# Kernel tuning notes

Measured on AMD Instinct MI355X. Metric: run time of the kernel, lower is better.

Reference implementation:

```python
import jax, jax.numpy as jnp
import numpy as np

EMBED = 64
HEAD = 16

def setup_inputs() -> dict:
    key = jax.random.key(0)
    k1, k2, k3, k4 = jax.random.split(key, 4)
    x = jax.random.normal(k1, (4, 4096, EMBED), dtype=jnp.float32)
    # store weights as [in, out] so forward is x @ W (equivalent to torch Linear with W.T)
    Wq = jax.random.normal(k2, (EMBED, HEAD), dtype=jnp.float32) * (1.0 / np.sqrt(EMBED))
    Wk = jax.random.normal(k3, (EMBED, HEAD), dtype=jnp.float32) * (1.0 / np.sqrt(EMBED))
    Wv = jax.random.normal(k4, (EMBED, EMBED), dtype=jnp.float32) * (1.0 / np.sqrt(EMBED))
    return {"x": x, "Wq": Wq, "Wk": Wk, "Wv": Wv}

def reference(x, Wq, Wk, Wv):
    # q,k: [B,T,HEAD]; v: [B,T,EMBED]
    q = x @ Wq
    k = x @ Wk
    v = x @ Wv
    scores = jnp.einsum('bqh,bkh->bqk', q, k)  # [B,T,T]
    T = scores.shape[-1]
    # causal mask: positions with key > query set to -inf BEFORE scaling (matches original; same result)
    causal = jnp.tril(jnp.ones((T, T), dtype=bool))
    scores = jnp.where(causal, scores, -jnp.inf)
    attn = jax.nn.softmax(scores / np.sqrt(HEAD).astype(np.float32), axis=-1)
    return jnp.einsum('bqk,bkd->bqd', attn, v)  # [B,T,EMBED]
```

## Files before the change

kernel.cpp:

```cpp
#include <hip/hip_runtime.h>


#define TSEQ 4096
#define NBATCH 4

typedef __attribute__((ext_vector_type(4)))  float fvec4;
typedef __attribute__((ext_vector_type(16))) float f32x16;
typedef __attribute__((ext_vector_type(4)))  short s16x4;
typedef __attribute__((ext_vector_type(8)))  short s16x8;

union I4S8 { int i[4]; s16x8 v; };

static __device__ __forceinline__ unsigned short f2bf(float f) {
    unsigned u = __float_as_uint(f);
    u += 0x7FFFu + ((u >> 16) & 1u);
    return (unsigned short)(u >> 16);
}

static __device__ __forceinline__ int cvt_pk_bf16(float lo, float hi) {
    int r;
    asm("v_cvt_pk_bf16_f32 %0, %1, %2" : "=v"(r) : "v"(lo), "v"(hi));
    return r;
}

static __device__ __forceinline__ s16x8 cat4(s16x4 a, s16x4 b) {
    return __builtin_shufflevector(a, b, 0, 1, 2, 3, 4, 5, 6, 7);
}

__global__ __launch_bounds__(128)
__attribute__((amdgpu_waves_per_eu(2, 4)))
void proj_kernel(
    const float* __restrict__ x,  const float* __restrict__ Wq,
    const float* __restrict__ Wk, const float* __restrict__ Wv,
    unsigned short* __restrict__ qb, unsigned short* __restrict__ kb,
    unsigned short* __restrict__ vf)
{
    __shared__ float xs[64][66];
    __shared__ __align__(16) unsigned short Wh[96][76], Wl[96][76];
    const int tid  = threadIdx.x;
    const int w    = tid >> 6;
    const int lane = tid & 63;
    const int col  = lane & 31;
    const int g    = lane >> 5;

    {
        const float* xblk = x + (size_t)blockIdx.x * 64 * 64;
        #pragma unroll
        for (int j = 0; j < 8; ++j) {
            const int fi = (tid + 128 * j) * 4;
            fvec4 v = *(const fvec4*)(xblk + fi);
            const int r = fi >> 6, c = fi & 63;
            xs[r][c + 0] = v[0]; xs[r][c + 1] = v[1];
            xs[r][c + 2] = v[2]; xs[r][c + 3] = v[3];
        }
    }
    const float SCQ = 0.25f * 1.44269504088896340736f;
    #pragma unroll
    for (int j = 0; j < 8; ++j) {
        const int idx = tid + 128 * j;
        const int n = idx & 15, k = idx >> 4;
        float wv = Wq[idx] * SCQ;
        unsigned short h = f2bf(wv);
        Wh[n][k] = h;
        Wl[n][k] = f2bf(wv - __uint_as_float((unsigned)h << 16));
    }
    #pragma unroll
    for (int j = 0; j < 8; ++j) {
        const int idx = tid + 128 * j;
        const int n = idx & 15, k = idx >> 4;
        float wv = Wk[idx];
        unsigned short h = f2bf(wv);
        Wh[16 + n][k] = h;
        Wl[16 + n][k] = f2bf(wv - __uint_as_float((unsigned)h << 16));
    }
    #pragma unroll
    for (int j = 0; j < 32; ++j) {
        const int idx = tid + 128 * j;
        const int n = idx & 63, k = idx >> 6;
        float wv = Wv[idx];
        unsigned short h = f2bf(wv);
        Wh[32 + n][k] = h;
        Wl[32 + n][k] = f2bf(wv - __uint_as_float((unsigned)h << 16));
    }
    __syncthreads();

    const int row0 = blockIdx.x * 64 + w * 32;
    const int lrow = w * 32 + col;

    s16x8 xh[4], xl[4];
    #pragma unroll
    for (int kc = 0; kc < 4; ++kc) {
        const float* xp = &xs[lrow][kc * 16 + 8 * g];
        float2 a0 = *(const float2*)(xp + 0);
        float2 a1 = *(const float2*)(xp + 2);
        float2 a2 = *(const float2*)(xp + 4);
        float2 a3 = *(const float2*)(xp + 6);
        I4S8 uh, ul;
        uh.i[0] = cvt_pk_bf16(a0.x, a0.y);
        uh.i[1] = cvt_pk_bf16(a1.x, a1.y);
        uh.i[2] = cvt_pk_bf16(a2.x, a2.y);
        uh.i[3] = cvt_pk_bf16(a3.x, a3.y);
        ul.i[0] = cvt_pk_bf16(a0.x - __uint_as_float((unsigned)uh.i[0] << 16),
                              a0.y - __uint_as_float((unsigned)uh.i[0] & 0xffff0000u));
        ul.i[1] = cvt_pk_bf16(a1.x - __uint_as_float((unsigned)uh.i[1] << 16),
                              a1.y - __uint_as_float((unsigned)uh.i[1] & 0xffff0000u));
        ul.i[2] = cvt_pk_bf16(a2.x - __uint_as_float((unsigned)uh.i[2] << 16),
                              a2.y - __uint_as_float((unsigned)uh.i[2] & 0xffff0000u));
        ul.i[3] = cvt_pk_bf16(a3.x - __uint_as_float((unsigned)uh.i[3] << 16),
                              a3.y - __uint_as_float((unsigned)uh.i[3] & 0xffff0000u));
        xh[kc] = uh.v; xl[kc] = ul.v;
    }

    f32x16 acc0 = (f32x16)0.0f, acc1 = (f32x16)0.0f, acc2 = (f32x16)0.0f;
    #pragma unroll
    for (int nt = 0; nt < 3; ++nt) {
        const int n = nt * 32 + col;
        f32x16 a = nt == 0 ? acc0 : (nt == 1 ? acc1 : acc2);
        #pragma unroll
        for (int kc = 0; kc < 4; ++kc) {
            const int off = kc * 16 + 8 * g;
            s16x8 bh = cat4(*(const s16x4*)&Wh[n][off], *(const s16x4*)&Wh[n][off + 4]);
            s16x8 bl = cat4(*(const s16x4*)&Wl[n][off], *(const s16x4*)&Wl[n][off + 4]);
            a = __builtin_amdgcn_mfma_f32_32x32x16_bf16(xh[kc], bh, a, 0, 0, 0);
            a = __builtin_amdgcn_mfma_f32_32x32x16_bf16(xl[kc], bh, a, 0, 0, 0);
            a = __builtin_amdgcn_mfma_f32_32x32x16_bf16(xh[kc], bl, a, 0, 0, 0);
        }
        if (nt == 0) acc0 = a; else if (nt == 1) acc1 = a; else acc2 = a;
    }

    {
        unsigned short* dst = (col < 16) ? (qb + col) : (kb + (col - 16));
        #pragma unroll
        for (int rr = 0; rr < 16; ++rr) {
            const int grow = row0 + (rr & 3) + 8 * (rr >> 2) + 4 * g;
            dst[(size_t)grow * 16] = f2bf(acc0[rr]);
        }
    }
    {
        unsigned short* const vtile = vf + (size_t)blockIdx.x * 4096;
        #pragma unroll
        for (int mt = 0; mt < 2; ++mt) {
            const f32x16 a = mt ? acc2 : acc1;
            #pragma unroll
            for (int ci = 0; ci < 2; ++ci) {
                I4S8 pk;
                pk.i[0] = cvt_pk_bf16(a[8*ci + 0], a[8*ci + 1]);
                pk.i[1] = cvt_pk_bf16(a[8*ci + 2], a[8*ci + 3]);
                pk.i[2] = cvt_pk_bf16(a[8*ci + 4], a[8*ci + 5]);
                pk.i[3] = cvt_pk_bf16(a[8*ci + 6], a[8*ci + 7]);
                const int c = 2 * w + ci;
                *(s16x8*)(vtile + ((c * 2 + mt) * 64 + lane) * 8) = pk.v;
            }
        }
    }
}

template<bool DIAG>
static __device__ __forceinline__ void do_tile32(
    const unsigned short* kp, const unsigned short* vt, const int lane,
    const s16x8 qf, const int col, const int g,
    f32x16& o0, f32x16& o1, float& lsum)
{
    s16x8 kf   = *(const s16x8*)(kp);
    s16x8 va00 = *(const s16x8*)(vt + (0 * 64 + lane) * 8);
    s16x8 va01 = *(const s16x8*)(vt + (1 * 64 + lane) * 8);
    s16x8 va10 = *(const s16x8*)(vt + (2 * 64 + lane) * 8);
    s16x8 va11 = *(const s16x8*)(vt + (3 * 64 + lane) * 8);

    f32x16 s = __builtin_amdgcn_mfma_f32_32x32x16_bf16(kf, qf, (f32x16)0.0f, 0, 0, 0);

    float psA = 0.f, psB = 0.f;
    #pragma unroll
    for (int rr = 0; rr < 16; ++rr) {
        float ev = __builtin_amdgcn_exp2f(s[rr]);
        if (DIAG) {
            const int drow = (rr & 3) + 8 * (rr >> 2) + 4 * g;
            ev = (drow <= col) ? ev : 0.f;
        }
        s[rr] = ev;
        if (rr & 1) psB += ev; else psA += ev;
    }
    lsum += psA + psB;

    I4S8 pa, pb;
    pa.i[0] = cvt_pk_bf16(s[0],  s[1]);
    pa.i[1] = cvt_pk_bf16(s[2],  s[3]);
    pa.i[2] = cvt_pk_bf16(s[4],  s[5]);
    pa.i[3] = cvt_pk_bf16(s[6],  s[7]);
    pb.i[0] = cvt_pk_bf16(s[8],  s[9]);
    pb.i[1] = cvt_pk_bf16(s[10], s[11]);
    pb.i[2] = cvt_pk_bf16(s[12], s[13]);
    pb.i[3] = cvt_pk_bf16(s[14], s[15]);

    o0 = __builtin_amdgcn_mfma_f32_32x32x16_bf16(va00, pa.v, o0, 0, 0, 0);
    o1 = __builtin_amdgcn_mfma_f32_32x32x16_bf16(va01, pa.v, o1, 0, 0, 0);
    o0 = __builtin_amdgcn_mfma_f32_32x32x16_bf16(va10, pb.v, o0, 0, 0, 0);
    o1 = __builtin_amdgcn_mfma_f32_32x32x16_bf16(va11, pb.v, o1, 0, 0, 0);
}

__global__ __launch_bounds__(1024)
__attribute__((amdgpu_num_vgpr(128), amdgpu_waves_per_eu(4, 4)))
void attn_kernel(
    const unsigned short* __restrict__ qb, const unsigned short* __restrict__ kb,
    const unsigned short* __restrict__ vf, float* __restrict__ out)
{
    __shared__ float pl[16][32];
    __shared__ float pO[2048 * 17];
    __shared__ float outS[32][66];

    const int tid  = threadIdx.x;
    const int w    = tid >> 6;
    const int lane = tid & 63;
    const int col  = lane & 31;
    const int g    = lane >> 5;
    const int b    = blockIdx.y;
    const int p    = blockIdx.x;

    const unsigned short* const kbase = kb + (size_t)b * TSEQ * 16 + (size_t)col * 16 + 8 * g;
    const unsigned short* const vbase = vf + (size_t)b * 64 * 4096;

    for (int half = 0; half < 2; ++half) {
        const int i  = half ? (127 - p) : p;
        const int q0 = i * 32;

        const s16x8 qf = *(const s16x8*)(qb + ((size_t)(b * TSEQ) + q0 + col) * 16 + 8 * g);

        f32x16 o0 = (f32x16)0.0f, o1 = (f32x16)0.0f;
        float lsum = 0.f;

        int t = w;
        for (; t < i; t += 16) {
            do_tile32<false>(kbase + (size_t)t * 512,
                             vbase + (size_t)(t >> 1) * 4096 + (t & 1) * 2048,
                             lane, qf, col, g, o0, o1, lsum);
        }
        if (t == i) {
            do_tile32<true>(kbase + (size_t)t * 512,
                            vbase + (size_t)(t >> 1) * 4096 + (t & 1) * 2048,
                            lane, qf, col, g, o0, o1, lsum);
        }
        lsum += __shfl_xor(lsum, 32);

        if (g == 0) pl[w][col] = lsum;
        #pragma unroll
        for (int mt = 0; mt < 2; ++mt) {
            const f32x16 oa = mt ? o1 : o0;
            #pragma unroll
            for (int rr = 0; rr < 16; ++rr) {
                const int dv = mt * 32 + (rr & 3) + 8 * (rr >> 2) + 4 * g;
                pO[(dv * 32 + col) * 17 + w] = oa[rr];
            }
        }
        __syncthreads();

        {
            const int q   = tid & 31;
            const int dvh = tid >> 5;
            float L = 0.f;
            #pragma unroll
            for (int ww = 0; ww < 16; ++ww) L += pl[ww][q];
            const float inv = 1.0f / L;
            #pragma unroll
            for (int pass = 0; pass < 2; ++pass) {
                const int dv = dvh + 32 * pass;
                const float* prow = &pO[(dv * 32 + q) * 17];
                float sA = 0.f, sB = 0.f;
                #pragma unroll
                for (int c = 0; c < 8; ++c) { sA += prow[2*c]; sB += prow[2*c+1]; }
                outS[q][dv] = (sA + sB) * inv;
            }
        }
        __syncthreads();

        {
            const int q2  = tid >> 5;
            const int dvp = (tid & 31) * 2;
            float2 v2 = *(const float2*)&outS[q2][dvp];
            *(float2*)(out + ((size_t)(b * TSEQ) + q0 + q2) * 64 + dvp) = v2;
        }
    }
}

extern "C" void kernel_launch(void* const* d_in, const int* in_sizes, int n_in,
                              void* d_out, int out_size, void* d_ws, size_t ws_size,
                              hipStream_t stream) {
    const float* x  = (const float*)d_in[0];
    const float* Wq = (const float*)d_in[1];
    const float* Wk = (const float*)d_in[2];
    const float* Wv = (const float*)d_in[3];

    unsigned short* qb = (unsigned short*)d_ws;
    unsigned short* kb = qb + (size_t)NBATCH * TSEQ * 16;
    unsigned short* vf = kb + (size_t)NBATCH * TSEQ * 16;
    float* out = (float*)d_out;

    proj_kernel<<<dim3((NBATCH * TSEQ) / 64), 128, 0, stream>>>(x, Wq, Wk, Wv, qb, kb, vf);
    attn_kernel<<<dim3(64, NBATCH), 1024, 0, stream>>>(qb, kb, vf, out);
}
```

Before: 24.15 us.

## Precompute split-bf16 weight fragments in a separate prep kernel

Adds a single-block wprep_kernel that converts Wq (pre-scaled), Wk and Wv into hi/lo bf16 pairs, stored in MFMA B-fragment order in workspace. The projection kernel then loads these fragments straight from global memory into registers. This removes the per-block weight conversion, the transposed LDS stores and the LDS reads, along with about 29KB of shared memory per block, which may raise occupancy. The cost is an extra kernel launch with a serial dependency and one more global read of the weights in every block.

```diff
diff --git a/kernel.cpp b/kernel.cpp
--- a/kernel.cpp
+++ b/kernel.cpp
@@ -23,20 +23,51 @@
     return r;
 }
 
-static __device__ __forceinline__ s16x8 cat4(s16x4 a, s16x4 b) {
-    return __builtin_shufflevector(a, b, 0, 1, 2, 3, 4, 5, 6, 7);
+__global__ __launch_bounds__(256) void wprep_kernel(
+    const float* __restrict__ Wq, const float* __restrict__ Wk,
+    const float* __restrict__ Wv,
+    unsigned short* __restrict__ whf, unsigned short* __restrict__ wlf)
+{
+    const float SCQ = 0.25f * 1.44269504088896340736f;
+    const int t = threadIdx.x;
+    #pragma unroll
+    for (int j = 0; j < 3; ++j) {
+        const int r  = t + 256 * j;
+        const int ch = r >> 6;
+        const int l  = r & 63;
+        const int nt = ch >> 2, kc = ch & 3;
+        const int n  = nt * 32 + (l & 31);
+        const int k0 = kc * 16 + (l >> 5) * 8;
+        float wv[8];
+        #pragma unroll
+        for (int e = 0; e < 8; ++e) {
+            const int k = k0 + e;
+            wv[e] = (nt == 0)
+                  ? ((n < 16) ? Wq[k * 16 + n] * SCQ : Wk[k * 16 + (n - 16)])
+                  : Wv[k * 64 + (nt - 1) * 32 + (l & 31)];
+        }
+        I4S8 hi, lo;
+        #pragma unroll
+        for (int ii = 0; ii < 4; ++ii) {
+            hi.i[ii] = cvt_pk_bf16(wv[2*ii], wv[2*ii + 1]);
+            const float h0 = __uint_as_float((unsigned)hi.i[ii] << 16);
+            const float h1 = __uint_as_float((unsigned)hi.i[ii] & 0xffff0000u);
+            lo.i[ii] = cvt_pk_bf16(wv[2*ii] - h0, wv[2*ii + 1] - h1);
+        }
+        *(s16x8*)(whf + (size_t)r * 8) = hi.v;
+        *(s16x8*)(wlf + (size_t)r * 8) = lo.v;
+    }
 }
 
 __global__ __launch_bounds__(128)
 __attribute__((amdgpu_waves_per_eu(2, 4)))
 void proj_kernel(
-    const float* __restrict__ x,  const float* __restrict__ Wq,
-    const float* __restrict__ Wk, const float* __restrict__ Wv,
+    const float* __restrict__ x,
+    const unsigned short* __restrict__ whf, const unsigned short* __restrict__ wlf,
     unsigned short* __restrict__ qb, unsigned short* __restrict__ kb,
     unsigned short* __restrict__ vf)
 {
     __shared__ float xs[64][66];
-    __shared__ __align__(16) unsigned short Wh[96][76], Wl[96][76];
     const int tid  = threadIdx.x;
     const int w    = tid >> 6;
     const int lane = tid & 63;
@@ -53,34 +84,6 @@
             xs[r][c + 0] = v[0]; xs[r][c + 1] = v[1];
             xs[r][c + 2] = v[2]; xs[r][c + 3] = v[3];
         }
-    }
-    const float SCQ = 0.25f * 1.44269504088896340736f;
-    #pragma unroll
-    for (int j = 0; j < 8; ++j) {
-        const int idx = tid + 128 * j;
-        const int n = idx & 15, k = idx >> 4;
-        float wv = Wq[idx] * SCQ;
-        unsigned short h = f2bf(wv);
-        Wh[n][k] = h;
-        Wl[n][k] = f2bf(wv - __uint_as_float((unsigned)h << 16));
-    }
-    #pragma unroll
-    for (int j = 0; j < 8; ++j) {
-        const int idx = tid + 128 * j;
-        const int n = idx & 15, k = idx >> 4;
-        float wv = Wk[idx];
-        unsigned short h = f2bf(wv);
-        Wh[16 + n][k] = h;
-        Wl[16 + n][k] = f2bf(wv - __uint_as_float((unsigned)h << 16));
-    }
-    #pragma unroll
-    for (int j = 0; j < 32; ++j) {
-        const int idx = tid + 128 * j;
-        const int n = idx & 63, k = idx >> 6;
-        float wv = Wv[idx];
-        unsigned short h = f2bf(wv);
-        Wh[32 + n][k] = h;
-        Wl[32 + n][k] = f2bf(wv - __uint_as_float((unsigned)h << 16));
     }
     __syncthreads();
 
@@ -114,16 +117,19 @@
     f32x16 acc0 = (f32x16)0.0f, acc1 = (f32x16)0.0f, acc2 = (f32x16)0.0f;
     #pragma unroll
     for (int nt = 0; nt < 3; ++nt) {
-        const int n = nt * 32 + col;
         f32x16 a = nt == 0 ? acc0 : (nt == 1 ? acc1 : acc2);
+        s16x8 bh[4], bl[4];
         #pragma unroll
         for (int kc = 0; kc < 4; ++kc) {
-            const int off = kc * 16 + 8 * g;
-            s16x8 bh = cat4(*(const s16x4*)&Wh[n][off], *(const s16x4*)&Wh[n][off + 4]);
-            s16x8 bl = cat4(*(const s16x4*)&Wl[n][off], *(const s16x4*)&Wl[n][off + 4]);
-            a = __builtin_amdgcn_mfma_f32_32x32x16_bf16(xh[kc], bh, a, 0, 0, 0);
-            a = __builtin_amdgcn_mfma_f32_32x32x16_bf16(xl[kc], bh, a, 0, 0, 0);
-            a = __builtin_amdgcn_mfma_f32_32x32x16_bf16(xh[kc], bl, a, 0, 0, 0);
+            const size_t fo = ((size_t)((nt * 4 + kc) * 64 + lane)) * 8;
+            bh[kc] = *(const s16x8*)(whf + fo);
+            bl[kc] = *(const s16x8*)(wlf + fo);
+        }
+        #pragma unroll
+        for (int kc = 0; kc < 4; ++kc) {
+            a = __builtin_amdgcn_mfma_f32_32x32x16_bf16(xh[kc], bh[kc], a, 0, 0, 0);
+            a = __builtin_amdgcn_mfma_f32_32x32x16_bf16(xl[kc], bh[kc], a, 0, 0, 0);
+            a = __builtin_amdgcn_mfma_f32_32x32x16_bf16(xh[kc], bl[kc], a, 0, 0, 0);
         }
         if (nt == 0) acc0 = a; else if (nt == 1) acc1 = a; else acc2 = a;
     }
@@ -289,11 +295,14 @@
     const float* Wk = (const float*)d_in[2];
     const float* Wv = (const float*)d_in[3];
 
-    unsigned short* qb = (unsigned short*)d_ws;
-    unsigned short* kb = qb + (size_t)NBATCH * TSEQ * 16;
-    unsigned short* vf = kb + (size_t)NBATCH * TSEQ * 16;
+    unsigned short* qb  = (unsigned short*)d_ws;
+    unsigned short* kb  = qb + (size_t)NBATCH * TSEQ * 16;
+    unsigned short* vf  = kb + (size_t)NBATCH * TSEQ * 16;
+    unsigned short* whf = vf + (size_t)NBATCH * 64 * 4096;
+    unsigned short* wlf = whf + 12 * 64 * 8;
     float* out = (float*)d_out;
 
-    proj_kernel<<<dim3((NBATCH * TSEQ) / 64), 128, 0, stream>>>(x, Wq, Wk, Wv, qb, kb, vf);
+    wprep_kernel<<<1, 256, 0, stream>>>(Wq, Wk, Wv, whf, wlf);
+    proj_kernel<<<dim3((NBATCH * TSEQ) / 64), 128, 0, stream>>>(x, whf, wlf, qb, kb, vf);
     attn_kernel<<<dim3(64, NBATCH), 1024, 0, stream>>>(qb, kb, vf, out);
 }
```

Result: slower. 27.63 us (+14.4%).

## Fuse projection and attention into one cooperative kernel with grid sync

Applied to the files above, without the earlier changes.

Merges the separate projection and attention kernels into a single cooperative launch of 256 blocks of 1024 threads. Each block first computes the bf16 Q/K/V projection for its 64 rows using 6 waves, then a grid-wide sync, then runs the attention phase. Shared memory is aliased between the two phases. This removes one kernel launch and the gap between launches, at the cost of a grid barrier, idle waves during projection, and a requirement that all blocks are co-resident.

```diff
diff --git a/kernel.cpp b/kernel.cpp
--- a/kernel.cpp
+++ b/kernel.cpp
@@ -1,4 +1,7 @@
 #include <hip/hip_runtime.h>
+#include <hip/hip_cooperative_groups.h>
+
+namespace cg = cooperative_groups;
 
 
 #define TSEQ 4096
@@ -25,134 +28,6 @@
 
 static __device__ __forceinline__ s16x8 cat4(s16x4 a, s16x4 b) {
     return __builtin_shufflevector(a, b, 0, 1, 2, 3, 4, 5, 6, 7);
-}
-
-__global__ __launch_bounds__(128)
-__attribute__((amdgpu_waves_per_eu(2, 4)))
-void proj_kernel(
-    const float* __restrict__ x,  const float* __restrict__ Wq,
-    const float* __restrict__ Wk, const float* __restrict__ Wv,
-    unsigned short* __restrict__ qb, unsigned short* __restrict__ kb,
-    unsigned short* __restrict__ vf)
-{
-    __shared__ float xs[64][66];
-    __shared__ __align__(16) unsigned short Wh[96][76], Wl[96][76];
-    const int tid  = threadIdx.x;
-    const int w    = tid >> 6;
-    const int lane = tid & 63;
-    const int col  = lane & 31;
-    const int g    = lane >> 5;
-
-    {
-        const float* xblk = x + (size_t)blockIdx.x * 64 * 64;
-        #pragma unroll
-        for (int j = 0; j < 8; ++j) {
-            const int fi = (tid + 128 * j) * 4;
-            fvec4 v = *(const fvec4*)(xblk + fi);
-            const int r = fi >> 6, c = fi & 63;
-            xs[r][c + 0] = v[0]; xs[r][c + 1] = v[1];
-            xs[r][c + 2] = v[2]; xs[r][c + 3] = v[3];
-        }
-    }
-    const float SCQ = 0.25f * 1.44269504088896340736f;
-    #pragma unroll
-    for (int j = 0; j < 8; ++j) {
-        const int idx = tid + 128 * j;
-        const int n = idx & 15, k = idx >> 4;
-        float wv = Wq[idx] * SCQ;
-        unsigned short h = f2bf(wv);
-        Wh[n][k] = h;
-        Wl[n][k] = f2bf(wv - __uint_as_float((unsigned)h << 16));
-    }
-    #pragma unroll
-    for (int j = 0; j < 8; ++j) {
-        const int idx = tid + 128 * j;
-        const int n = idx & 15, k = idx >> 4;
-        float wv = Wk[idx];
-        unsigned short h = f2bf(wv);
-        Wh[16 + n][k] = h;
-        Wl[16 + n][k] = f2bf(wv - __uint_as_float((unsigned)h << 16));
-    }
-    #pragma unroll
-    for (int j = 0; j < 32; ++j) {
-        const int idx = tid + 128 * j;
-        const int n = idx & 63, k = idx >> 6;
-        float wv = Wv[idx];
-        unsigned short h = f2bf(wv);
-        Wh[32 + n][k] = h;
-        Wl[32 + n][k] = f2bf(wv - __uint_as_float((unsigned)h << 16));
-    }
-    __syncthreads();
-
-    const int row0 = blockIdx.x * 64 + w * 32;
-    const int lrow = w * 32 + col;
-
-    s16x8 xh[4], xl[4];
-    #pragma unroll
-    for (int kc = 0; kc < 4; ++kc) {
-        const float* xp = &xs[lrow][kc * 16 + 8 * g];
-        float2 a0 = *(const float2*)(xp + 0);
-        float2 a1 = *(const float2*)(xp + 2);
-        float2 a2 = *(const float2*)(xp + 4);
-        float2 a3 = *(const float2*)(xp + 6);
-        I4S8 uh, ul;
-        uh.i[0] = cvt_pk_bf16(a0.x, a0.y);
-        uh.i[1] = cvt_pk_bf16(a1.x, a1.y);
-        uh.i[2] = cvt_pk_bf16(a2.x, a2.y);
-        uh.i[3] = cvt_pk_bf16(a3.x, a3.y);
-        ul.i[0] = cvt_pk_bf16(a0.x - __uint_as_float((unsigned)uh.i[0] << 16),
-                              a0.y - __uint_as_float((unsigned)uh.i[0] & 0xffff0000u));
-        ul.i[1] = cvt_pk_bf16(a1.x - __uint_as_float((unsigned)uh.i[1] << 16),
-                              a1.y - __uint_as_float((unsigned)uh.i[1] & 0xffff0000u));
-        ul.i[2] = cvt_pk_bf16(a2.x - __uint_as_float((unsigned)uh.i[2] << 16),
-                              a2.y - __uint_as_float((unsigned)uh.i[2] & 0xffff0000u));
-        ul.i[3] = cvt_pk_bf16(a3.x - __uint_as_float((unsigned)uh.i[3] << 16),
-                              a3.y - __uint_as_float((unsigned)uh.i[3] & 0xffff0000u));
-        xh[kc] = uh.v; xl[kc] = ul.v;
-    }
-
-    f32x16 acc0 = (f32x16)0.0f, acc1 = (f32x16)0.0f, acc2 = (f32x16)0.0f;
-    #pragma unroll
-    for (int nt = 0; nt < 3; ++nt) {
-        const int n = nt * 32 + col;
-        f32x16 a = nt == 0 ? acc0 : (nt == 1 ? acc1 : acc2);
-        #pragma unroll
-        for (int kc = 0; kc < 4; ++kc) {
-            const int off = kc * 16 + 8 * g;
-            s16x8 bh = cat4(*(const s16x4*)&Wh[n][off], *(const s16x4*)&Wh[n][off + 4]);
-            s16x8 bl = cat4(*(const s16x4*)&Wl[n][off], *(const s16x4*)&Wl[n][off + 4]);
-            a = __builtin_amdgcn_mfma_f32_32x32x16_bf16(xh[kc], bh, a, 0, 0, 0);
-            a = __builtin_amdgcn_mfma_f32_32x32x16_bf16(xl[kc], bh, a, 0, 0, 0);
-            a = __builtin_amdgcn_mfma_f32_32x32x16_bf16(xh[kc], bl, a, 0, 0, 0);
-        }
-        if (nt == 0) acc0 = a; else if (nt == 1) acc1 = a; else acc2 = a;
-    }
-
-    {
-        unsigned short* dst = (col < 16) ? (qb + col) : (kb + (col - 16));
-        #pragma unroll
-        for (int rr = 0; rr < 16; ++rr) {
-            const int grow = row0 + (rr & 3) + 8 * (rr >> 2) + 4 * g;
-            dst[(size_t)grow * 16] = f2bf(acc0[rr]);
-        }
-    }
-    {
-        unsigned short* const vtile = vf + (size_t)blockIdx.x * 4096;
-        #pragma unroll
-        for (int mt = 0; mt < 2; ++mt) {
-            const f32x16 a = mt ? acc2 : acc1;
-            #pragma unroll
-            for (int ci = 0; ci < 2; ++ci) {
-                I4S8 pk;
-                pk.i[0] = cvt_pk_bf16(a[8*ci + 0], a[8*ci + 1]);
-                pk.i[1] = cvt_pk_bf16(a[8*ci + 2], a[8*ci + 3]);
-                pk.i[2] = cvt_pk_bf16(a[8*ci + 4], a[8*ci + 5]);
-                pk.i[3] = cvt_pk_bf16(a[8*ci + 6], a[8*ci + 7]);
-                const int c = 2 * w + ci;
-                *(s16x8*)(vtile + ((c * 2 + mt) * 64 + lane) * 8) = pk.v;
-            }
-        }
-    }
 }
 
 template<bool DIAG>
@@ -200,21 +75,130 @@
 
 __global__ __launch_bounds__(1024)
 __attribute__((amdgpu_num_vgpr(128), amdgpu_waves_per_eu(4, 4)))
-void attn_kernel(
-    const unsigned short* __restrict__ qb, const unsigned short* __restrict__ kb,
-    const unsigned short* __restrict__ vf, float* __restrict__ out)
+void fused_kernel(
+    const float* __restrict__ x,  const float* __restrict__ Wq,
+    const float* __restrict__ Wk, const float* __restrict__ Wv,
+    unsigned short* __restrict__ qb, unsigned short* __restrict__ kb,
+    unsigned short* __restrict__ vf, float* __restrict__ out)
 {
-    __shared__ float pl[16][32];
-    __shared__ float pO[2048 * 17];
-    __shared__ float outS[32][66];
-
+    __shared__ __align__(16) char smem[149760];
+    float* const pl   = (float*)smem;
+    float* const pO   = (float*)(smem + 2048);
+    float* const outS = (float*)(smem + 141312);
+    float (*const xs)[66]          = (float(*)[66])smem;
+    unsigned short (*const Wh)[76] = (unsigned short(*)[76])(smem + 16896);
+    unsigned short (*const Wl)[76] = (unsigned short(*)[76])(smem + 31488);
+
+    const int bid  = blockIdx.x;
     const int tid  = threadIdx.x;
     const int w    = tid >> 6;
     const int lane = tid & 63;
     const int col  = lane & 31;
     const int g    = lane >> 5;
-    const int b    = blockIdx.y;
-    const int p    = blockIdx.x;
+
+    {
+        const float* xblk = x + (size_t)bid * 64 * 64;
+        const int fi = tid * 4;
+        fvec4 v = *(const fvec4*)(xblk + fi);
+        const int r = fi >> 6, c = fi & 63;
+        xs[r][c + 0] = v[0]; xs[r][c + 1] = v[1];
+        xs[r][c + 2] = v[2]; xs[r][c + 3] = v[3];
+    }
+    const float SCQ = 0.25f * 1.44269504088896340736f;
+    {
+        const int n = tid & 15, k = tid >> 4;
+        float wv = Wq[tid] * SCQ;
+        unsigned short h = f2bf(wv);
+        Wh[n][k] = h;
+        Wl[n][k] = f2bf(wv - __uint_as_float((unsigned)h << 16));
+    }
+    {
+        const int n = tid & 15, k = tid >> 4;
+        float wv = Wk[tid];
+        unsigned short h = f2bf(wv);
+        Wh[16 + n][k] = h;
+        Wl[16 + n][k] = f2bf(wv - __uint_as_float((unsigned)h << 16));
+    }
+    #pragma unroll
+    for (int j = 0; j < 4; ++j) {
+        const int idx = tid + 1024 * j;
+        const int n = idx & 63, k = idx >> 6;
+        float wv = Wv[idx];
+        unsigned short h = f2bf(wv);
+        Wh[32 + n][k] = h;
+        Wl[32 + n][k] = f2bf(wv - __uint_as_float((unsigned)h << 16));
+    }
+    __syncthreads();
+
+    if (w < 6) {
+        const int nt = w >> 1;
+        const int rh = w & 1;
+        const int row0 = bid * 64 + rh * 32;
+        const int lrow = rh * 32 + col;
+
+        s16x8 xh[4], xl[4];
+        #pragma unroll
+        for (int kc = 0; kc < 4; ++kc) {
+            const float* xp = &xs[lrow][kc * 16 + 8 * g];
+            float2 a0 = *(const float2*)(xp + 0);
+            float2 a1 = *(const float2*)(xp + 2);
+            float2 a2 = *(const float2*)(xp + 4);
+            float2 a3 = *(const float2*)(xp + 6);
+            I4S8 uh, ul;
+            uh.i[0] = cvt_pk_bf16(a0.x, a0.y);
+            uh.i[1] = cvt_pk_bf16(a1.x, a1.y);
+            uh.i[2] = cvt_pk_bf16(a2.x, a2.y);
+            uh.i[3] = cvt_pk_bf16(a3.x, a3.y);
+            ul.i[0] = cvt_pk_bf16(a0.x - __uint_as_float((unsigned)uh.i[0] << 16),
+                                  a0.y - __uint_as_float((unsigned)uh.i[0] & 0xffff0000u));
+            ul.i[1] = cvt_pk_bf16(a1.x - __uint_as_float((unsigned)uh.i[1] << 16),
+                                  a1.y - __uint_as_float((unsigned)uh.i[1] & 0xffff0000u));
+            ul.i[2] = cvt_pk_bf16(a2.x - __uint_as_float((unsigned)uh.i[2] << 16),
+                                  a2.y - __uint_as_float((unsigned)uh.i[2] & 0xffff0000u));
+            ul.i[3] = cvt_pk_bf16(a3.x - __uint_as_float((unsigned)uh.i[3] << 16),
+                                  a3.y - __uint_as_float((unsigned)uh.i[3] & 0xffff0000u));
+            xh[kc] = uh.v; xl[kc] = ul.v;
+        }
+
+        f32x16 acc = (f32x16)0.0f;
+        const int n = nt * 32 + col;
+        #pragma unroll
+        for (int kc = 0; kc < 4; ++kc) {
+            const int off = kc * 16 + 8 * g;
+            s16x8 bh = cat4(*(const s16x4*)&Wh[n][off], *(const s16x4*)&Wh[n][off + 4]);
+            s16x8 bl = cat4(*(const s16x4*)&Wl[n][off], *(const s16x4*)&Wl[n][off + 4]);
+            acc = __builtin_amdgcn_mfma_f32_32x32x16_bf16(xh[kc], bh, acc, 0, 0, 0);
+            acc = __builtin_amdgcn_mfma_f32_32x32x16_bf16(xl[kc], bh, acc, 0, 0, 0);
+            acc = __builtin_amdgcn_mfma_f32_32x32x16_bf16(xh[kc], bl, acc, 0, 0, 0);
+        }
+
+        if (nt == 0) {
+            unsigned short* dst = (col < 16) ? (qb + col) : (kb + (col - 16));
+            #pragma unroll
+            for (int rr = 0; rr < 16; ++rr) {
+                const int grow = row0 + (rr & 3) + 8 * (rr >> 2) + 4 * g;
+                dst[(size_t)grow * 16] = f2bf(acc[rr]);
+            }
+        } else {
+            const int mt = nt - 1;
+            unsigned short* const vtile = vf + (size_t)bid * 4096;
+            #pragma unroll
+            for (int ci = 0; ci < 2; ++ci) {
+                I4S8 pk;
+                pk.i[0] = cvt_pk_bf16(acc[8*ci + 0], acc[8*ci + 1]);
+                pk.i[1] = cvt_pk_bf16(acc[8*ci + 2], acc[8*ci + 3]);
+                pk.i[2] = cvt_pk_bf16(acc[8*ci + 4], acc[8*ci + 5]);
+                pk.i[3] = cvt_pk_bf16(acc[8*ci + 6], acc[8*ci + 7]);
+                const int c = 2 * rh + ci;
+                *(s16x8*)(vtile + ((c * 2 + mt) * 64 + lane) * 8) = pk.v;
+            }
+        }
+    }
+
+    cg::this_grid().sync();
+
+    const int b = bid >> 6;
+    const int p = bid & 63;
 
     const unsigned short* const kbase = kb + (size_t)b * TSEQ * 16 + (size_t)col * 16 + 8 * g;
     const unsigned short* const vbase = vf + (size_t)b * 64 * 4096;
@@ -241,7 +225,8 @@
         }
         lsum += __shfl_xor(lsum, 32);
 
-        if (g == 0) pl[w][col] = lsum;
+        __syncthreads();
+        if (g == 0) pl[w * 32 + col] = lsum;
         #pragma unroll
         for (int mt = 0; mt < 2; ++mt) {
             const f32x16 oa = mt ? o1 : o0;
@@ -258,7 +243,7 @@
             const int dvh = tid >> 5;
             float L = 0.f;
             #pragma unroll
-            for (int ww = 0; ww < 16; ++ww) L += pl[ww][q];
+            for (int ww = 0; ww < 16; ++ww) L += pl[ww * 32 + q];
             const float inv = 1.0f / L;
             #pragma unroll
             for (int pass = 0; pass < 2; ++pass) {
@@ -267,7 +252,7 @@
                 float sA = 0.f, sB = 0.f;
                 #pragma unroll
                 for (int c = 0; c < 8; ++c) { sA += prow[2*c]; sB += prow[2*c+1]; }
-                outS[q][dv] = (sA + sB) * inv;
+                outS[q * 66 + dv] = (sA + sB) * inv;
             }
         }
         __syncthreads();
@@ -275,7 +260,7 @@
         {
             const int q2  = tid >> 5;
             const int dvp = (tid & 31) * 2;
-            float2 v2 = *(const float2*)&outS[q2][dvp];
+            float2 v2 = *(const float2*)&outS[q2 * 66 + dvp];
             *(float2*)(out + ((size_t)(b * TSEQ) + q0 + q2) * 64 + dvp) = v2;
         }
     }
@@ -294,6 +279,8 @@
     unsigned short* vf = kb + (size_t)NBATCH * TSEQ * 16;
     float* out = (float*)d_out;
 
-    proj_kernel<<<dim3((NBATCH * TSEQ) / 64), 128, 0, stream>>>(x, Wq, Wk, Wv, qb, kb, vf);
-    attn_kernel<<<dim3(64, NBATCH), 1024, 0, stream>>>(qb, kb, vf, out);
-}
+    void* args[] = {(void*)&x, (void*)&Wq, (void*)&Wk, (void*)&Wv,
+                    (void*)&qb, (void*)&kb, (void*)&vf, (void*)&out};
+    hipLaunchCooperativeKernel((const void*)fused_kernel,
+                               dim3(NBATCH * 64), dim3(1024), args, 0, stream);
+}
```

Result: slower. 62.99 us (+160.9%).
